# Performance work log

Hardware: AMD Instinct MI355X
Metric: run time of the kernel (lower is better)

The kernel has to match this reference:

```python
import jax, jax.numpy as jnp
import numpy as np

R_EARTH_KM = 6371.0

def haversine(lat1, lon1, lat2, lon2):
    # inputs in degrees, output distance in km
    lat1, lon1, lat2, lon2 = (jnp.radians(x) for x in (lat1, lon1, lat2, lon2))
    dlat = lat2 - lat1
    dlon = lon2 - lon1
    a = jnp.sin(dlat * 0.5) ** 2 + jnp.cos(lat1) * jnp.cos(lat2) * jnp.sin(dlon * 0.5) ** 2
    return 2.0 * R_EARTH_KM * jnp.arcsin(jnp.sqrt(jnp.clip(a, 0.0, 1.0)))

def _latlon(key, n):
    k1, k2 = jax.random.split(key)
    lat = jax.random.uniform(k1, (n,), minval=-90.0, maxval=90.0)
    lon = jax.random.uniform(k2, (n,), minval=-180.0, maxval=180.0)
    return jnp.stack([lat, lon], axis=1).astype(jnp.float32)

def setup_inputs() -> dict:
    key = jax.random.key(0)
    ks = jax.random.split(key, 12)
    B, D = 4096, 1792
    NC, NM, NF = 3000, 7000, 13000
    scale = 0.02
    return {
        'features': jax.random.normal(ks[0], (B, D), dtype=jnp.float32),
        'labels_2d': _latlon(ks[1], B),
        'coarse_partition': _latlon(ks[2], NC),
        'middle_partition': _latlon(ks[3], NM),
        'fine_partition': _latlon(ks[4], NF),
        'middle_parents': jax.random.randint(ks[5], (NM,), 0, NC, dtype=jnp.int32),
        'fine_parents': jax.random.randint(ks[6], (NF,), 0, NM, dtype=jnp.int32),
        'coarse_w': jax.random.normal(ks[7], (D, NC), dtype=jnp.float32) * scale,
        'coarse_b': jnp.zeros((NC,), dtype=jnp.float32),
        'middle_w': jax.random.normal(ks[8], (D, NM), dtype=jnp.float32) * scale,
        'middle_b': jnp.zeros((NM,), dtype=jnp.float32),
        'fine_w': jax.random.normal(ks[9], (D, NF), dtype=jnp.float32) * scale,
        'fine_b': jnp.zeros((NF,), dtype=jnp.float32),
    }

def _single_loss(labels_2d, logits, partition):
    # cartesian-product haversine cdist: [B, M]
    dists = haversine(labels_2d[:, 0:1], labels_2d[:, 1:2],
                      partition[None, :, 0], partition[None, :, 1])
    labels_index = jnp.argmin(dists, axis=1)
    logp = jax.nn.log_softmax(logits, axis=1)
    nll = -jnp.take_along_axis(logp, labels_index[:, None], axis=1)[:, 0]
    return jnp.mean(nll)

def reference(features, labels_2d, coarse_partition, middle_partition, fine_partition,
              middle_parents, fine_parents, coarse_w, coarse_b, middle_w, middle_b,
              fine_w, fine_b):
    coarse_logits = features @ coarse_w + coarse_b
    middle_logits = features @ middle_w + middle_b
    fine_logits = features @ fine_w + fine_b

    loss = (_single_loss(labels_2d, coarse_logits, coarse_partition)
            + _single_loss(labels_2d, middle_logits, middle_partition)
            + _single_loss(labels_2d, fine_logits, fine_partition))

    fine_probs = jax.nn.softmax(fine_logits, axis=1)
    middle_probs = jax.nn.softmax(middle_logits, axis=1)
    coarse_probs = jax.nn.softmax(coarse_logits, axis=1)
    # hierarchy combine: gather parent probs and multiply
    final_probs = (fine_probs
                   * middle_probs[:, fine_parents]
                   * coarse_probs[:, middle_parents[fine_parents]])

    predictions = fine_partition[jnp.argmax(final_probs, axis=1)]  # [B, 2]
    d = haversine(labels_2d[:, 0], labels_2d[:, 1], predictions[:, 0], predictions[:, 1])
    thresholds = jnp.array([1.0, 25.0, 200.0, 750.0, 2500.0], dtype=jnp.float32)
    acc = jnp.mean((d[None, :] <= thresholds[:, None]).astype(jnp.float32), axis=1)
    return loss, acc
```

## Files before the change

kernel.cpp:

```cpp
#include <hip/hip_runtime.h>
#include <hip/hip_fp16.h>
#include <math.h>

#define B_   4096
#define D_   1792
#define NC_  3000
#define NM_  7000
#define NF_  13000
#define NCP  3072
#define NMP  7168
#define NFP  13312
#define NTOT (NCP + NMP + NFP)
#define OFFC 0
#define OFFM NCP
#define OFFF (NCP + NMP)
#define WROWS 8192
#define DEG2RAD 0.017453292519943295f

typedef _Float16 half8  __attribute__((ext_vector_type(8)));
typedef _Float16 half4v __attribute__((ext_vector_type(4)));
typedef float    f32x4  __attribute__((ext_vector_type(4)));

__device__ __forceinline__ void async16(const void* g, void* l) {
  __builtin_amdgcn_global_load_lds(
      (const __attribute__((address_space(1))) void*)g,
      (__attribute__((address_space(3))) void*)l, 16, 0, 0);
}

__global__ void prep_kernel(const float* __restrict__ labels,
                            const float* __restrict__ cp, const float* __restrict__ mp,
                            const float* __restrict__ fp,
                            const float* __restrict__ cb, const float* __restrict__ mb,
                            const float* __restrict__ fb,
                            float* __restrict__ bias, float4* __restrict__ ptrig,
                            float4* __restrict__ ltrig, float* __restrict__ accum) {
  int i = blockIdx.x * 256 + threadIdx.x;
  if (i < NTOT) {
    float v = 0.f;
    if (i < OFFM)      { if (i < NC_) v = cb[i]; }
    else if (i < OFFF) { int j = i - OFFM; if (j < NM_) v = mb[j]; }
    else               { int j = i - OFFF; if (j < NF_) v = fb[j]; }
    bias[i] = v;
  }
  if (i < NC_ + NM_ + NF_) {
    const float* src; int j = i;
    if (i < NC_)            { src = cp; }
    else if (i < NC_ + NM_) { src = mp; j = i - NC_; }
    else                    { src = fp; j = i - NC_ - NM_; }
    float la = src[2 * j] * DEG2RAD, lo = src[2 * j + 1] * DEG2RAD;
    float sla, cla, slo, clo;
    sincosf(la, &sla, &cla); sincosf(lo, &slo, &clo);
    ptrig[i] = make_float4(sla, cla, slo, clo);
  }
  if (i < B_) {
    float la = labels[2 * i] * DEG2RAD, lo = labels[2 * i + 1] * DEG2RAD;
    float sla, cla, slo, clo;
    sincosf(la, &sla, &cla); sincosf(lo, &slo, &clo);
    ltrig[i] = make_float4(sla, cla, slo, clo);
  }
  if (i < 64) accum[i] = 0.f;
}

__global__ void cvt_feat(const float4* __restrict__ in, half4v* __restrict__ out) {
  int i = blockIdx.x * 256 + threadIdx.x;
  float4 v = in[i];
  half4v h;
  h[0] = (_Float16)v.x; h[1] = (_Float16)v.y; h[2] = (_Float16)v.z; h[3] = (_Float16)v.w;
  out[i] = h;
}

__global__ void transpose_w(const float* __restrict__ w, _Float16* __restrict__ wt,
                            int Nfull, int c0, int ntrue_chunk) {
  __shared__ float tile[32][33];
  int n0 = blockIdx.x * 32, k0 = blockIdx.y * 32;
  int tx = threadIdx.x, ty = threadIdx.y;
#pragma unroll
  for (int i = 0; i < 4; ++i) {
    int kk = ty + i * 8;
    int n = n0 + tx;
    float v = (n < ntrue_chunk) ? w[(size_t)(k0 + kk) * Nfull + c0 + n] : 0.f;
    tile[kk][tx] = v;
  }
  __syncthreads();
#pragma unroll
  for (int i = 0; i < 4; ++i) {
    int nn = ty + i * 8;
    wt[(size_t)(n0 + nn) * D_ + k0 + tx] = (_Float16)tile[tx][nn];
  }
}

__global__ void argmin_kernel(const float4* __restrict__ ptrig, const float4* __restrict__ ltrig,
                              int* __restrict__ lidx) {
  __shared__ float rv[256];
  __shared__ int ri[256];
  int b = blockIdx.x, tid = threadIdx.x;
  float4 lt = ltrig[b];
  const int base[3] = {0, NC_, NC_ + NM_};
  const int cnt[3]  = {NC_, NM_, NF_};
#pragma unroll
  for (int h = 0; h < 3; ++h) {
    float best = 1e30f; int bi = 0;
    for (int i = tid; i < cnt[h]; i += 256) {
      float4 pt = ptrig[base[h] + i];
      float cdla = lt.y * pt.y + lt.x * pt.x;
      float cdlo = lt.w * pt.w + lt.z * pt.z;
      float a = 0.5f * (1.f - cdla) + (lt.y * pt.y) * 0.5f * (1.f - cdlo);
      if (a < best) { best = a; bi = i; }
    }
    rv[tid] = best; ri[tid] = bi;
    __syncthreads();
    for (int o = 128; o; o >>= 1) {
      if (tid < o) {
        if (rv[tid + o] < rv[tid] || (rv[tid + o] == rv[tid] && ri[tid + o] < ri[tid])) {
          rv[tid] = rv[tid + o]; ri[tid] = ri[tid + o];
        }
      }
      __syncthreads();
    }
    if (tid == 0) lidx[h * B_ + b] = ri[0];
    __syncthreads();
  }
}

__global__ __launch_bounds__(512, 2) void gemm_f16(const _Float16* __restrict__ A,
                                                   const _Float16* __restrict__ Bt,
                                                   const float* __restrict__ bias,
                                                   _Float16* __restrict__ C, int coff) {
  __shared__ _Float16 lds[65536];
  const int tid = threadIdx.x;
  const int lane = tid & 63, w = tid >> 6;
  const int wm = w & 1, wn = w >> 1;
  const int q = lane >> 4, l15 = lane & 15;
  const int q8 = gridDim.x >> 3;
  const int bxr = blockIdx.x;
  const int bx = (bxr & 7) * q8 + (bxr >> 3);
  const int mt = bx & 15, nt = bx >> 4;
  const int m0 = mt * 256;
  const int nl0 = nt * 256;
  const int gn0 = coff + nl0;

  f32x4 acc[8][4];
#pragma unroll
  for (int a = 0; a < 8; ++a)
#pragma unroll
    for (int b2 = 0; b2 < 4; ++b2) acc[a][b2] = (f32x4){0.f, 0.f, 0.f, 0.f};

  const int amB = (wm * 128 + l15) * 32;
  const int bnB = (wn * 64 + l15) * 32;
  const int xsl = ((q ^ ((l15 >> 1) & 3)) << 3);
  const int kbl = (lane & 3) ^ ((lane >> 3) & 3);
  const int rr = lane >> 2;

  auto stageP = [&](int r, int P) {
    const int kk = P * 32 + kbl * 8;
#pragma unroll
    for (int j = 0; j < 2; ++j) {
      int seg = w * 2 + j;
      async16(A  + (size_t)(m0  + seg * 16 + rr) * D_ + kk,
              (void*)(lds + r * 8192 + seg * 512));
      async16(Bt + (size_t)(nl0 + seg * 16 + rr) * D_ + kk,
              (void*)(lds + 32768 + r * 8192 + seg * 512));
    }
  };

  half8 af[8], bf[4];

#define PHASE(RS, RN, WAITSTR, DOSTAGE, PST) { \
    if (DOSTAGE) stageP(RS, PST); \
    __builtin_amdgcn_s_setprio(1); \
    _Pragma("unroll") for (int tm = 0; tm < 8; ++tm) { \
      _Pragma("unroll") for (int tn = 0; tn < 4; ++tn) \
        acc[tm][tn] = __builtin_amdgcn_mfma_f32_16x16x32_f16(af[tm], bf[tn], acc[tm][tn], 0, 0, 0); \
      af[tm] = *(const half8*)(lds + (RN) * 8192 + amB + tm * 512 + xsl); \
    } \
    __builtin_amdgcn_s_setprio(0); \
    _Pragma("unroll") for (int tn = 0; tn < 4; ++tn) \
      bf[tn] = *(const half8*)(lds + 32768 + (RN) * 8192 + bnB + tn * 512 + xsl); \
    asm volatile(WAITSTR ::: "memory"); \
    __builtin_amdgcn_sched_barrier(0); \
    __builtin_amdgcn_s_barrier(); }

  stageP(0, 0); stageP(1, 1); stageP(2, 2); stageP(3, 3);
  asm volatile("s_waitcnt vmcnt(8)" ::: "memory");
  __builtin_amdgcn_sched_barrier(0);
  __builtin_amdgcn_s_barrier();
#pragma unroll
  for (int tm = 0; tm < 8; ++tm)
    af[tm] = *(const half8*)(lds + amB + tm * 512 + xsl);
#pragma unroll
  for (int tn = 0; tn < 4; ++tn)
    bf[tn] = *(const half8*)(lds + 32768 + bnB + tn * 512 + xsl);
  asm volatile("s_waitcnt lgkmcnt(0)" ::: "memory");
  __builtin_amdgcn_sched_barrier(0);
  __builtin_amdgcn_s_barrier();

#pragma unroll 1
  for (int i = 0; i < 13; ++i) {
    const int P0 = 4 * i;
    PHASE(0, 1, "s_waitcnt vmcnt(8) lgkmcnt(0)", true, P0 + 4);
    PHASE(1, 2, "s_waitcnt vmcnt(8) lgkmcnt(0)", true, P0 + 5);
    PHASE(2, 3, "s_waitcnt vmcnt(8) lgkmcnt(0)", true, P0 + 6);
    PHASE(3, 0, "s_waitcnt vmcnt(8) lgkmcnt(0)", true, P0 + 7);
  }
  PHASE(0, 1, "s_waitcnt vmcnt(4) lgkmcnt(0)", false, 0);
  PHASE(0, 2, "s_waitcnt vmcnt(0) lgkmcnt(0)", false, 0);
  {
    __builtin_amdgcn_s_setprio(1);
#pragma unroll
    for (int tm = 0; tm < 8; ++tm) {
#pragma unroll
      for (int tn = 0; tn < 4; ++tn)
        acc[tm][tn] = __builtin_amdgcn_mfma_f32_16x16x32_f16(af[tm], bf[tn], acc[tm][tn], 0, 0, 0);
      af[tm] = *(const half8*)(lds + 3 * 8192 + amB + tm * 512 + xsl);
    }
    __builtin_amdgcn_s_setprio(0);
#pragma unroll
    for (int tn = 0; tn < 4; ++tn)
      bf[tn] = *(const half8*)(lds + 32768 + 3 * 8192 + bnB + tn * 512 + xsl);
  }
  {
    __builtin_amdgcn_s_setprio(1);
#pragma unroll
    for (int tm = 0; tm < 8; ++tm)
#pragma unroll
      for (int tn = 0; tn < 4; ++tn)
        acc[tm][tn] = __builtin_amdgcn_mfma_f32_16x16x32_f16(af[tm], bf[tn], acc[tm][tn], 0, 0, 0);
    __builtin_amdgcn_s_setprio(0);
  }
#undef PHASE

  float bn[4];
#pragma unroll
  for (int tn = 0; tn < 4; ++tn) bn[tn] = bias[gn0 + wn * 64 + tn * 16 + l15];
#pragma unroll
  for (int tm = 0; tm < 8; ++tm) {
    int gm = m0 + wm * 128 + tm * 16 + q * 4;
#pragma unroll
    for (int tn = 0; tn < 4; ++tn) {
      int gn = gn0 + wn * 64 + tn * 16 + l15;
      _Float16* dst = C + (size_t)gm * NTOT + gn;
#pragma unroll
      for (int r = 0; r < 4; ++r) dst[(size_t)r * NTOT] = (_Float16)(acc[tm][tn][r] + bn[tn]);
    }
  }
}

__device__ __forceinline__ float block_lse(float m, float s, float* ms, float* ss, int tid) {
  ms[tid] = m; ss[tid] = s;
  __syncthreads();
  for (int o = 128; o; o >>= 1) {
    if (tid < o) {
      float m2 = ms[tid + o], s2 = ss[tid + o];
      if (m2 > ms[tid]) { ss[tid] = s2 + ss[tid] * __expf(ms[tid] - m2); ms[tid] = m2; }
      else ss[tid] += s2 * __expf(m2 - ms[tid]);
    }
    __syncthreads();
  }
  float r = ms[0] + logf(ss[0]);
  __syncthreads();
  return r;
}

__global__ __launch_bounds__(256) void final_kernel(const _Float16* __restrict__ logits,
                                                    const int* __restrict__ mpar,
                                                    const int* __restrict__ fpar,
                                                    const float4* __restrict__ ptrig,
                                                    const float4* __restrict__ ltrig,
                                                    const int* __restrict__ lidx,
                                                    float* __restrict__ nll_buf,
                                                    float* __restrict__ accum) {
  __shared__ float co[NC_];
  __shared__ float par[NM_];
  __shared__ float ms[256], ss[256];
  __shared__ int ri[256];
  int b = blockIdx.x, tid = threadIdx.x;
  const _Float16* row = logits + (size_t)b * NTOT;

  float m = -1e30f, s = 0.f;
  {
    const half8* rc = (const half8*)(row + OFFC);
    for (int i = tid; i < NC_ / 8; i += 256) {
      half8 v = rc[i];
      float x[8];
#pragma unroll
      for (int j = 0; j < 8; ++j) x[j] = (float)v[j];
      float vm = fmaxf(fmaxf(fmaxf(x[0], x[1]), fmaxf(x[2], x[3])),
                       fmaxf(fmaxf(x[4], x[5]), fmaxf(x[6], x[7])));
      if (vm > m) { s *= __expf(m - vm); m = vm; }
#pragma unroll
      for (int j = 0; j < 8; ++j) s += __expf(x[j] - m);
      f32x4 lo = {x[0], x[1], x[2], x[3]}, hi = {x[4], x[5], x[6], x[7]};
      *(f32x4*)(co + i * 8)     = lo;
      *(f32x4*)(co + i * 8 + 4) = hi;
    }
  }
  float lseC = block_lse(m, s, ms, ss, tid);

  m = -1e30f; s = 0.f;
  {
    const half8* rm = (const half8*)(row + OFFM);
    const int4* mp4 = (const int4*)mpar;
    for (int i = tid; i < NM_ / 8; i += 256) {
      half8 v = rm[i];
      int4 p0 = mp4[2 * i], p1 = mp4[2 * i + 1];
      float x[8];
#pragma unroll
      for (int j = 0; j < 8; ++j) x[j] = (float)v[j];
      float vm = fmaxf(fmaxf(fmaxf(x[0], x[1]), fmaxf(x[2], x[3])),
                       fmaxf(fmaxf(x[4], x[5]), fmaxf(x[6], x[7])));
      if (vm > m) { s *= __expf(m - vm); m = vm; }
#pragma unroll
      for (int j = 0; j < 8; ++j) s += __expf(x[j] - m);
      int pj[8] = {p0.x, p0.y, p0.z, p0.w, p1.x, p1.y, p1.z, p1.w};
      f32x4 lo = {x[0] + co[pj[0]], x[1] + co[pj[1]], x[2] + co[pj[2]], x[3] + co[pj[3]]};
      f32x4 hi = {x[4] + co[pj[4]], x[5] + co[pj[5]], x[6] + co[pj[6]], x[7] + co[pj[7]]};
      *(f32x4*)(par + i * 8)     = lo;
      *(f32x4*)(par + i * 8 + 4) = hi;
    }
  }
  float lseM = block_lse(m, s, ms, ss, tid);

  m = -1e30f; s = 0.f;
  float best = -1e30f; int bi = 0;
  {
    const half8* rf = (const half8*)(row + OFFF);
    const int4* fp4 = (const int4*)fpar;
    for (int i = tid; i < NF_ / 8; i += 256) {
      half8 v = rf[i];
      int4 p0 = fp4[2 * i], p1 = fp4[2 * i + 1];
      float x[8];
#pragma unroll
      for (int j = 0; j < 8; ++j) x[j] = (float)v[j];
      float vm = fmaxf(fmaxf(fmaxf(x[0], x[1]), fmaxf(x[2], x[3])),
                       fmaxf(fmaxf(x[4], x[5]), fmaxf(x[6], x[7])));
      if (vm > m) { s *= __expf(m - vm); m = vm; }
#pragma unroll
      for (int j = 0; j < 8; ++j) s += __expf(x[j] - m);
      int pj[8] = {p0.x, p0.y, p0.z, p0.w, p1.x, p1.y, p1.z, p1.w};
#pragma unroll
      for (int j = 0; j < 8; ++j) {
        float vv = x[j] + par[pj[j]];
        if (vv > best) { best = vv; bi = i * 8 + j; }
      }
    }
  }
  float lseF = block_lse(m, s, ms, ss, tid);

  ms[tid] = best; ri[tid] = bi;
  __syncthreads();
  for (int o = 128; o; o >>= 1) {
    if (tid < o) {
      if (ms[tid + o] > ms[tid] || (ms[tid + o] == ms[tid] && ri[tid + o] < ri[tid])) {
        ms[tid] = ms[tid + o]; ri[tid] = ri[tid + o];
      }
    }
    __syncthreads();
  }

  if (tid == 0) {
    int ic = lidx[b], im = lidx[B_ + b], ifn = lidx[2 * B_ + b];
    nll_buf[b] = (lseC - (float)row[OFFC + ic])
               + (lseM - (float)row[OFFM + im])
               + (lseF - (float)row[OFFF + ifn]);
    float4 pt = ptrig[NC_ + NM_ + ri[0]];
    float4 lt = ltrig[b];
    float cdla = lt.y * pt.y + lt.x * pt.x;
    float cdlo = lt.w * pt.w + lt.z * pt.z;
    float a = 0.5f * (1.f - cdla) + (lt.y * pt.y) * 0.5f * (1.f - cdlo);
    a = fminf(fmaxf(a, 0.f), 1.f);
    float d = 2.f * 6371.f * asinf(sqrtf(a));
    const float thr[5] = {1.f, 25.f, 200.f, 750.f, 2500.f};
#pragma unroll
    for (int j = 0; j < 5; ++j)
      if (d <= thr[j]) atomicAdd(accum + 1 + j, 1.f);
  }
}

__global__ void finish_kernel(const float* __restrict__ accum,
                              const float* __restrict__ nll, float* __restrict__ out) {
  __shared__ float sh[256];
  int tid = threadIdx.x;
  float s = 0.f;
  for (int i = tid; i < B_; i += 256) s += nll[i];
  sh[tid] = s;
  __syncthreads();
  for (int o = 128; o; o >>= 1) { if (tid < o) sh[tid] += sh[tid + o]; __syncthreads(); }
  if (tid == 0) out[0] = sh[0] * (1.f / 4096.f);
  if (tid >= 1 && tid < 6) out[tid] = accum[tid] * (1.f / 4096.f);
}

extern "C" void kernel_launch(void* const* d_in, const int* in_sizes, int n_in,
                              void* d_out, int out_size, void* d_ws, size_t ws_size,
                              hipStream_t stream) {
  (void)in_sizes; (void)n_in; (void)out_size; (void)ws_size;
  const float* features = (const float*)d_in[0];
  const float* labels   = (const float*)d_in[1];
  const float* cpart    = (const float*)d_in[2];
  const float* mpart    = (const float*)d_in[3];
  const float* fpart    = (const float*)d_in[4];
  const int*   mpar     = (const int*)d_in[5];
  const int*   fpar     = (const int*)d_in[6];
  const float* cw       = (const float*)d_in[7];
  const float* cb       = (const float*)d_in[8];
  const float* mw       = (const float*)d_in[9];
  const float* mb       = (const float*)d_in[10];
  const float* fw       = (const float*)d_in[11];
  const float* fb       = (const float*)d_in[12];
  float* out = (float*)d_out;

  char* ws = (char*)d_ws;
  size_t off = 0;
  auto alloc = [&](size_t bytes) {
    char* p = ws + off;
    off += (bytes + 255) & ~(size_t)255;
    return p;
  };
  _Float16* feat16 = (_Float16*)alloc((size_t)B_ * D_ * 2);
  _Float16* wTbuf  = (_Float16*)alloc((size_t)WROWS * D_ * 2);
  _Float16* logits = (_Float16*)alloc((size_t)B_ * NTOT * 2);
  float*    bias   = (float*)alloc((size_t)NTOT * 4);
  float4*   ptrig  = (float4*)alloc((size_t)(NC_ + NM_ + NF_) * 16);
  float4*   ltrig  = (float4*)alloc((size_t)B_ * 16);
  int*      lidx   = (int*)alloc((size_t)3 * B_ * 4);
  float*    nll    = (float*)alloc((size_t)B_ * 4);
  float*    accum  = (float*)alloc(64 * 4);

  prep_kernel<<<dim3(NTOT / 256), dim3(256), 0, stream>>>(labels, cpart, mpart, fpart,
                                                          cb, mb, fb, bias, ptrig, ltrig, accum);
  cvt_feat<<<dim3(B_ * D_ / 4 / 256), dim3(256), 0, stream>>>((const float4*)features,
                                                              (half4v*)feat16);
  argmin_kernel<<<dim3(B_), dim3(256), 0, stream>>>(ptrig, ltrig, lidx);

  transpose_w<<<dim3(3072 / 32, D_ / 32), dim3(32, 8), 0, stream>>>(cw, wTbuf, NC_, 0, NC_);
  transpose_w<<<dim3(5120 / 32, D_ / 32), dim3(32, 8), 0, stream>>>(mw, wTbuf + (size_t)3072 * D_, NM_, 0, 5120);
  gemm_f16<<<dim3(512), dim3(512), 0, stream>>>(feat16, wTbuf, bias, logits, 0);

  transpose_w<<<dim3(2048 / 32, D_ / 32), dim3(32, 8), 0, stream>>>(mw, wTbuf, NM_, 5120, NM_ - 5120);
  transpose_w<<<dim3(6144 / 32, D_ / 32), dim3(32, 8), 0, stream>>>(fw, wTbuf + (size_t)2048 * D_, NF_, 0, 6144);
  gemm_f16<<<dim3(512), dim3(512), 0, stream>>>(feat16, wTbuf, bias, logits, 8192);

  transpose_w<<<dim3(7168 / 32, D_ / 32), dim3(32, 8), 0, stream>>>(fw, wTbuf, NF_, 6144, NF_ - 6144);
  gemm_f16<<<dim3(448), dim3(512), 0, stream>>>(feat16, wTbuf, bias, logits, 16384);

  final_kernel<<<dim3(B_), dim3(256), 0, stream>>>(logits, mpar, fpar, ptrig, ltrig,
                                                   lidx, nll, accum);
  finish_kernel<<<dim3(1), dim3(256), 0, stream>>>(accum, nll, out);
}
```

Before: 748.6 us.

## Fuse label argmin into final kernel, use wave-shuffle reductions, 512 threads

Removes the separate argmin kernel and computes the nearest-partition label indices inside the final per-row kernel. The shared-memory tree reductions are replaced with wavefront shuffle reductions plus a small cross-wave step. The final kernel now runs 512 threads per block, and the online-softmax max update becomes branchless. This saves one launch and the lidx round trip through global memory, and shortens reduction sync chains. In exchange the final kernel carries more work and a larger block, which may change occupancy.

```diff
diff --git a/kernel.cpp b/kernel.cpp
--- a/kernel.cpp
+++ b/kernel.cpp
@@ -86,39 +86,6 @@
   for (int i = 0; i < 4; ++i) {
     int nn = ty + i * 8;
     wt[(size_t)(n0 + nn) * D_ + k0 + tx] = (_Float16)tile[tx][nn];
-  }
-}
-
-__global__ void argmin_kernel(const float4* __restrict__ ptrig, const float4* __restrict__ ltrig,
-                              int* __restrict__ lidx) {
-  __shared__ float rv[256];
-  __shared__ int ri[256];
-  int b = blockIdx.x, tid = threadIdx.x;
-  float4 lt = ltrig[b];
-  const int base[3] = {0, NC_, NC_ + NM_};
-  const int cnt[3]  = {NC_, NM_, NF_};
-#pragma unroll
-  for (int h = 0; h < 3; ++h) {
-    float best = 1e30f; int bi = 0;
-    for (int i = tid; i < cnt[h]; i += 256) {
-      float4 pt = ptrig[base[h] + i];
-      float cdla = lt.y * pt.y + lt.x * pt.x;
-      float cdlo = lt.w * pt.w + lt.z * pt.z;
-      float a = 0.5f * (1.f - cdla) + (lt.y * pt.y) * 0.5f * (1.f - cdlo);
-      if (a < best) { best = a; bi = i; }
-    }
-    rv[tid] = best; ri[tid] = bi;
-    __syncthreads();
-    for (int o = 128; o; o >>= 1) {
-      if (tid < o) {
-        if (rv[tid + o] < rv[tid] || (rv[tid + o] == rv[tid] && ri[tid + o] < ri[tid])) {
-          rv[tid] = rv[tid + o]; ri[tid] = ri[tid + o];
-        }
-      }
-      __syncthreads();
-    }
-    if (tid == 0) lidx[h * B_ + b] = ri[0];
-    __syncthreads();
   }
 }
 
@@ -245,48 +212,120 @@
   }
 }
 
-__device__ __forceinline__ float block_lse(float m, float s, float* ms, float* ss, int tid) {
-  ms[tid] = m; ss[tid] = s;
-  __syncthreads();
-  for (int o = 128; o; o >>= 1) {
-    if (tid < o) {
-      float m2 = ms[tid + o], s2 = ss[tid + o];
-      if (m2 > ms[tid]) { ss[tid] = s2 + ss[tid] * __expf(ms[tid] - m2); ms[tid] = m2; }
-      else ss[tid] += s2 * __expf(m2 - ms[tid]);
-    }
-    __syncthreads();
-  }
-  float r = ms[0] + logf(ss[0]);
+__device__ __forceinline__ void lse_comb(float& m, float& s, float m2, float s2) {
+  float mn = fmaxf(m, m2);
+  s = s * __expf(m - mn) + s2 * __expf(m2 - mn);
+  m = mn;
+}
+
+__device__ __forceinline__ float block_lse(float m, float s, float* sm, float* ss, int tid) {
+#pragma unroll
+  for (int o = 32; o; o >>= 1)
+    lse_comb(m, s, __shfl_xor(m, o), __shfl_xor(s, o));
+  if ((tid & 63) == 0) { sm[tid >> 6] = m; ss[tid >> 6] = s; }
+  __syncthreads();
+  if (tid < 64) {
+    m = sm[tid & 7]; s = ss[tid & 7];
+#pragma unroll
+    for (int o = 4; o; o >>= 1)
+      lse_comb(m, s, __shfl_xor(m, o), __shfl_xor(s, o));
+    if (tid == 0) sm[0] = m + logf(s);
+  }
+  __syncthreads();
+  float r = sm[0];
   __syncthreads();
   return r;
 }
 
-__global__ __launch_bounds__(256) void final_kernel(const _Float16* __restrict__ logits,
+__device__ __forceinline__ int block_imin(float v, int idx, float* sv, int* si, int tid) {
+#pragma unroll
+  for (int o = 32; o; o >>= 1) {
+    float v2 = __shfl_xor(v, o); int i2 = __shfl_xor(idx, o);
+    if (v2 < v || (v2 == v && i2 < idx)) { v = v2; idx = i2; }
+  }
+  if ((tid & 63) == 0) { sv[tid >> 6] = v; si[tid >> 6] = idx; }
+  __syncthreads();
+  if (tid < 64) {
+    v = sv[tid & 7]; idx = si[tid & 7];
+#pragma unroll
+    for (int o = 4; o; o >>= 1) {
+      float v2 = __shfl_xor(v, o); int i2 = __shfl_xor(idx, o);
+      if (v2 < v || (v2 == v && i2 < idx)) { v = v2; idx = i2; }
+    }
+    if (tid == 0) si[0] = idx;
+  }
+  __syncthreads();
+  int r = si[0];
+  __syncthreads();
+  return r;
+}
+
+__device__ __forceinline__ int block_imax(float v, int idx, float* sv, int* si, int tid) {
+#pragma unroll
+  for (int o = 32; o; o >>= 1) {
+    float v2 = __shfl_xor(v, o); int i2 = __shfl_xor(idx, o);
+    if (v2 > v || (v2 == v && i2 < idx)) { v = v2; idx = i2; }
+  }
+  if ((tid & 63) == 0) { sv[tid >> 6] = v; si[tid >> 6] = idx; }
+  __syncthreads();
+  if (tid < 64) {
+    v = sv[tid & 7]; idx = si[tid & 7];
+#pragma unroll
+    for (int o = 4; o; o >>= 1) {
+      float v2 = __shfl_xor(v, o); int i2 = __shfl_xor(idx, o);
+      if (v2 > v || (v2 == v && i2 < idx)) { v = v2; idx = i2; }
+    }
+    if (tid == 0) si[0] = idx;
+  }
+  __syncthreads();
+  int r = si[0];
+  __syncthreads();
+  return r;
+}
+
+__global__ __launch_bounds__(512) void final_kernel(const _Float16* __restrict__ logits,
                                                     const int* __restrict__ mpar,
                                                     const int* __restrict__ fpar,
                                                     const float4* __restrict__ ptrig,
                                                     const float4* __restrict__ ltrig,
-                                                    const int* __restrict__ lidx,
                                                     float* __restrict__ nll_buf,
                                                     float* __restrict__ accum) {
   __shared__ float co[NC_];
   __shared__ float par[NM_];
-  __shared__ float ms[256], ss[256];
-  __shared__ int ri[256];
+  __shared__ float sv[8], sw[8];
+  __shared__ int   si[8];
   int b = blockIdx.x, tid = threadIdx.x;
   const _Float16* row = logits + (size_t)b * NTOT;
+  float4 lt = ltrig[b];
+
+  int lab[3];
+  const int hbase[3] = {0, NC_, NC_ + NM_};
+  const int hcnt[3]  = {NC_, NM_, NF_};
+#pragma unroll
+  for (int h = 0; h < 3; ++h) {
+    float best = 1e30f; int bi = 0;
+    for (int i = tid; i < hcnt[h]; i += 512) {
+      float4 pt = ptrig[hbase[h] + i];
+      float cdla = lt.y * pt.y + lt.x * pt.x;
+      float cdlo = lt.w * pt.w + lt.z * pt.z;
+      float a = 0.5f * (1.f - cdla) + (lt.y * pt.y) * 0.5f * (1.f - cdlo);
+      if (a < best) { best = a; bi = i; }
+    }
+    lab[h] = block_imin(best, bi, sv, si, tid);
+  }
 
   float m = -1e30f, s = 0.f;
   {
     const half8* rc = (const half8*)(row + OFFC);
-    for (int i = tid; i < NC_ / 8; i += 256) {
+    for (int i = tid; i < NC_ / 8; i += 512) {
       half8 v = rc[i];
       float x[8];
 #pragma unroll
       for (int j = 0; j < 8; ++j) x[j] = (float)v[j];
       float vm = fmaxf(fmaxf(fmaxf(x[0], x[1]), fmaxf(x[2], x[3])),
                        fmaxf(fmaxf(x[4], x[5]), fmaxf(x[6], x[7])));
-      if (vm > m) { s *= __expf(m - vm); m = vm; }
+      float mn = fmaxf(m, vm);
+      s *= __expf(m - mn); m = mn;
 #pragma unroll
       for (int j = 0; j < 8; ++j) s += __expf(x[j] - m);
       f32x4 lo = {x[0], x[1], x[2], x[3]}, hi = {x[4], x[5], x[6], x[7]};
@@ -294,13 +333,13 @@
       *(f32x4*)(co + i * 8 + 4) = hi;
     }
   }
-  float lseC = block_lse(m, s, ms, ss, tid);
+  float lseC = block_lse(m, s, sv, sw, tid);
 
   m = -1e30f; s = 0.f;
   {
     const half8* rm = (const half8*)(row + OFFM);
     const int4* mp4 = (const int4*)mpar;
-    for (int i = tid; i < NM_ / 8; i += 256) {
+    for (int i = tid; i < NM_ / 8; i += 512) {
       half8 v = rm[i];
       int4 p0 = mp4[2 * i], p1 = mp4[2 * i + 1];
       float x[8];
@@ -308,7 +347,8 @@
       for (int j = 0; j < 8; ++j) x[j] = (float)v[j];
       float vm = fmaxf(fmaxf(fmaxf(x[0], x[1]), fmaxf(x[2], x[3])),
                        fmaxf(fmaxf(x[4], x[5]), fmaxf(x[6], x[7])));
-      if (vm > m) { s *= __expf(m - vm); m = vm; }
+      float mn = fmaxf(m, vm);
+      s *= __expf(m - mn); m = mn;
 #pragma unroll
       for (int j = 0; j < 8; ++j) s += __expf(x[j] - m);
       int pj[8] = {p0.x, p0.y, p0.z, p0.w, p1.x, p1.y, p1.z, p1.w};
@@ -318,14 +358,14 @@
       *(f32x4*)(par + i * 8 + 4) = hi;
     }
   }
-  float lseM = block_lse(m, s, ms, ss, tid);
+  float lseM = block_lse(m, s, sv, sw, tid);
 
   m = -1e30f; s = 0.f;
   float best = -1e30f; int bi = 0;
   {
     const half8* rf = (const half8*)(row + OFFF);
     const int4* fp4 = (const int4*)fpar;
-    for (int i = tid; i < NF_ / 8; i += 256) {
+    for (int i = tid; i < NF_ / 8; i += 512) {
       half8 v = rf[i];
       int4 p0 = fp4[2 * i], p1 = fp4[2 * i + 1];
       float x[8];
@@ -333,7 +373,8 @@
       for (int j = 0; j < 8; ++j) x[j] = (float)v[j];
       float vm = fmaxf(fmaxf(fmaxf(x[0], x[1]), fmaxf(x[2], x[3])),
                        fmaxf(fmaxf(x[4], x[5]), fmaxf(x[6], x[7])));
-      if (vm > m) { s *= __expf(m - vm); m = vm; }
+      float mn = fmaxf(m, vm);
+      s *= __expf(m - mn); m = mn;
 #pragma unroll
       for (int j = 0; j < 8; ++j) s += __expf(x[j] - m);
       int pj[8] = {p0.x, p0.y, p0.z, p0.w, p1.x, p1.y, p1.z, p1.w};
@@ -344,26 +385,14 @@
       }
     }
   }
-  float lseF = block_lse(m, s, ms, ss, tid);
-
-  ms[tid] = best; ri[tid] = bi;
-  __syncthreads();
-  for (int o = 128; o; o >>= 1) {
-    if (tid < o) {
-      if (ms[tid + o] > ms[tid] || (ms[tid + o] == ms[tid] && ri[tid + o] < ri[tid])) {
-        ms[tid] = ms[tid + o]; ri[tid] = ri[tid + o];
-      }
-    }
-    __syncthreads();
-  }
+  float lseF = block_lse(m, s, sv, sw, tid);
+  int fbest = block_imax(best, bi, sv, si, tid);
 
   if (tid == 0) {
-    int ic = lidx[b], im = lidx[B_ + b], ifn = lidx[2 * B_ + b];
-    nll_buf[b] = (lseC - (float)row[OFFC + ic])
-               + (lseM - (float)row[OFFM + im])
-               + (lseF - (float)row[OFFF + ifn]);
-    float4 pt = ptrig[NC_ + NM_ + ri[0]];
-    float4 lt = ltrig[b];
+    nll_buf[b] = (lseC - (float)row[OFFC + lab[0]])
+               + (lseM - (float)row[OFFM + lab[1]])
+               + (lseF - (float)row[OFFF + lab[2]]);
+    float4 pt = ptrig[NC_ + NM_ + fbest];
     float cdla = lt.y * pt.y + lt.x * pt.x;
     float cdlo = lt.w * pt.w + lt.z * pt.z;
     float a = 0.5f * (1.f - cdla) + (lt.y * pt.y) * 0.5f * (1.f - cdlo);
@@ -421,7 +450,6 @@
   float*    bias   = (float*)alloc((size_t)NTOT * 4);
   float4*   ptrig  = (float4*)alloc((size_t)(NC_ + NM_ + NF_) * 16);
   float4*   ltrig  = (float4*)alloc((size_t)B_ * 16);
-  int*      lidx   = (int*)alloc((size_t)3 * B_ * 4);
   float*    nll    = (float*)alloc((size_t)B_ * 4);
   float*    accum  = (float*)alloc(64 * 4);
 
@@ -429,7 +457,6 @@
                                                           cb, mb, fb, bias, ptrig, ltrig, accum);
   cvt_feat<<<dim3(B_ * D_ / 4 / 256), dim3(256), 0, stream>>>((const float4*)features,
                                                               (half4v*)feat16);
-  argmin_kernel<<<dim3(B_), dim3(256), 0, stream>>>(ptrig, ltrig, lidx);
 
   transpose_w<<<dim3(3072 / 32, D_ / 32), dim3(32, 8), 0, stream>>>(cw, wTbuf, NC_, 0, NC_);
   transpose_w<<<dim3(5120 / 32, D_ / 32), dim3(32, 8), 0, stream>>>(mw, wTbuf + (size_t)3072 * D_, NM_, 0, 5120);
@@ -442,7 +469,7 @@
   transpose_w<<<dim3(7168 / 32, D_ / 32), dim3(32, 8), 0, stream>>>(fw, wTbuf, NF_, 6144, NF_ - 6144);
   gemm_f16<<<dim3(448), dim3(512), 0, stream>>>(feat16, wTbuf, bias, logits, 16384);
 
-  final_kernel<<<dim3(B_), dim3(256), 0, stream>>>(logits, mpar, fpar, ptrig, ltrig,
-                                                   lidx, nll, accum);
+  final_kernel<<<dim3(B_), dim3(512), 0, stream>>>(logits, mpar, fpar, ptrig, ltrig,
+                                                   nll, accum);
   finish_kernel<<<dim3(1), dim3(256), 0, stream>>>(accum, nll, out);
 }
```

Measured after the change: 751.0 us. About the same (+0.3%).
